# Kernel optimization log

Hardware: AMD Instinct MI355X
Metric: run time of the kernel (lower is better)

Reference implementation:

```python
import jax, jax.numpy as jnp
import numpy as np

B, C, H, W = 64, 256, 28, 28
EPS = 1e-8  # torch CosineSimilarity eps


def _make_grids(key):
    # coordinate meshgrid [2, H, W]: channel 0 = y, channel 1 = x
    yy, xx = jnp.meshgrid(jnp.arange(H, dtype=jnp.float32),
                          jnp.arange(W, dtype=jnp.float32), indexing='ij')
    coords = jnp.stack([yy, xx])  # [2, H, W]
    k1, k2 = jax.random.split(key)
    scale = jax.random.uniform(k1, (B, 1, 1, 1), minval=0.9, maxval=1.1)
    shift = jax.random.uniform(k2, (B, 2, 1, 1), minval=0.0, maxval=5.0)
    return coords[None] * scale + shift  # [B, 2, H, W]


def setup_inputs() -> dict:
    key = jax.random.key(0)
    ks = jax.random.split(key, 6)
    return {
        'y1': jax.random.normal(ks[0], (B, C, H, W), jnp.float32),
        'y2': jax.random.normal(ks[1], (B, C, H, W), jnp.float32),
        'z1': jax.random.normal(ks[2], (B, C, H, W), jnp.float32),
        'z2': jax.random.normal(ks[3], (B, C, H, W), jnp.float32),
        'view1_grid': _make_grids(ks[4]),
        'view2_grid': _make_grids(ks[5]),
    }


def _grid_distances(grid1, grid2):
    # grid*: [B, 2, H, W] -> [B, 2, N]; pairwise euclidean dist [B, N, N]
    g1 = grid1.reshape(grid1.shape[0], 2, -1)
    g2 = grid2.reshape(grid2.shape[0], 2, -1)
    dy = g1[:, 0, :, None] - g2[:, 0, None, :]
    dx = g1[:, 1, :, None] - g2[:, 1, None, :]
    return jnp.sqrt(dy * dy + dx * dx)


def _cosine_sim_pairwise(a, b):
    # a, b: [B, C, N]; cosine sim over channel dim -> [B, N, N]
    num = jnp.einsum('bcn,bcm->bnm', a, b)
    na = jnp.linalg.norm(a, axis=1)  # [B, N]
    nb = jnp.linalg.norm(b, axis=1)  # [B, N]
    den = jnp.maximum(na[:, :, None] * nb[:, None, :], EPS)
    return num / den


def _masked_mean(sim, mask):
    m = mask.astype(sim.dtype)
    return jnp.sum(sim * m) / jnp.sum(m)


def reference(y1, y2, z1, z2, view1_grid, view2_grid):
    distance_thr = 0.7
    y1f = y1.reshape(y1.shape[0], y1.shape[1], -1)
    y2f = y2.reshape(y2.shape[0], y2.shape[1], -1)
    z1f = z1.reshape(z1.shape[0], z1.shape[1], -1)
    z2f = z2.reshape(z2.shape[0], z2.shape[1], -1)

    distances = _grid_distances(view1_grid, view2_grid)  # [B, N, N]
    view1_bin = jnp.linalg.norm(view1_grid[..., 1, 1] - view1_grid[..., 0, 0], axis=-1)  # [B]
    view2_bin = jnp.linalg.norm(view2_grid[..., 1, 1] - view2_grid[..., 0, 0], axis=-1)  # [B]

    view1_mask = (distances / view1_bin[:, None, None]) <= distance_thr
    view2_mask = (distances / view2_bin[:, None, None]) <= distance_thr

    view1_loss = _masked_mean(_cosine_sim_pairwise(y1f, z2f), view1_mask)
    view2_loss = _masked_mean(_cosine_sim_pairwise(y2f, z1f), view2_mask)
    return -1.0 * (view1_loss + view2_loss)
```

## Files before the change

### kernel.cpp

```cpp
#include <hip/hip_runtime.h>
#include <hip/hip_bf16.h>

#define BB   64
#define CC   256
#define NPIX 784
#define BNP  (BB * NPIX)
#define SLOTS 128

__global__ __launch_bounds__(256) void transpose_k(
    const float* __restrict__ y1, const float* __restrict__ y2,
    const float* __restrict__ z1, const float* __restrict__ z2,
    float* __restrict__ o1, float* __restrict__ o2,
    float* __restrict__ o3, float* __restrict__ o4,
    float* __restrict__ nrm2) {
    int bx = blockIdx.x;
    int nt = bx % 13;
    int t  = bx / 13;
    int ct = t & 3;   t >>= 2;
    int b  = t & 63;
    int arr = t >> 6;

    const float* in = (arr == 0) ? y1 : (arr == 1) ? y2 : (arr == 2) ? z1 : z2;
    float* outp     = (arr == 0) ? o1 : (arr == 1) ? o2 : (arr == 2) ? o3 : o4;

    __shared__ float tile[64][65];

    int tid = threadIdx.x;
    int hi  = tid >> 4;
    int lo  = tid & 15;
    int n0  = nt * 64;
    int c0  = ct * 64;
    const float* inb = in + (size_t)b * (CC * NPIX);

#pragma unroll
    for (int k = 0; k < 4; k++) {
        int c = c0 + hi + 16 * k;
        int n = n0 + 4 * lo;
        float4 v = {0.f, 0.f, 0.f, 0.f};
        if (n < NPIX) v = *(const float4*)(inb + (size_t)c * NPIX + n);
        tile[hi + 16 * k][4 * lo + 0] = v.x;
        tile[hi + 16 * k][4 * lo + 1] = v.y;
        tile[hi + 16 * k][4 * lo + 2] = v.z;
        tile[hi + 16 * k][4 * lo + 3] = v.w;
    }
    __syncthreads();

    float* nrow = nrm2 + ((size_t)arr * BB + b) * NPIX;
#pragma unroll
    for (int k = 0; k < 4; k++) {
        int nl = hi + 16 * k;
        int n  = n0 + nl;
        float4 v;
        v.x = tile[4 * lo + 0][nl];
        v.y = tile[4 * lo + 1][nl];
        v.z = tile[4 * lo + 2][nl];
        v.w = tile[4 * lo + 3][nl];
        bool ok = (n < NPIX);
        if (ok)
            *(float4*)(outp + ((size_t)b * NPIX + n) * CC + c0 + 4 * lo) = v;
        float p = fmaf(v.x, v.x, fmaf(v.y, v.y, fmaf(v.z, v.z, v.w * v.w)));
#pragma unroll
        for (int off = 1; off < 16; off <<= 1) p += __shfl_xor(p, off);
        if (ok && lo == 0) atomicAdd(&nrow[n], p);
    }
}

__global__ __launch_bounds__(256) void pairs_k(
    const float* __restrict__ yt1, const float* __restrict__ yt2,
    const float* __restrict__ zt1, const float* __restrict__ zt2,
    const float* __restrict__ g1g, const float* __restrict__ g2g,
    const float* __restrict__ nrm2, double* __restrict__ acc) {
    int lane = threadIdx.x & 63;
    int w    = threadIdx.x >> 6;
    int wg   = blockIdx.x * 4 + w;
    int loss = (wg >= BNP) ? 1 : 0;
    int rem  = wg - loss * BNP;
    int b    = rem / NPIX;
    int i    = rem - b * NPIX;

    const float* g1 = g1g + (size_t)b * 2 * NPIX;
    const float* g2 = g2g + (size_t)b * 2 * NPIX;

    float g1y = g1[i];
    float g1x = g1[NPIX + i];

    const float* gb = loss ? g2 : g1;
    float d0  = gb[29] - gb[0];
    float d1  = gb[NPIX + 29] - gb[NPIX];
    float bin = __fsqrt_rn(__fadd_rn(__fmul_rn(d0, d0), __fmul_rn(d1, d1)));

    float t2y = g2[0], t2x = g2[NPIX];
    float s2y = g2[28] - g2[0];
    float s2x = g2[NPIX + 1] - g2[NPIX];
    float r  = 0.7f * bin * 1.0002f + 1e-4f;
    float cy = (g1y - t2y) / s2y;
    float cx = (g1x - t2x) / s2x;
    float ry = r / s2y + 0.05f;
    float rx = r / s2x + 0.05f;
    int jy0 = max(0,  (int)ceilf(cy - ry));
    int jy1 = min(27, (int)floorf(cy + ry));
    int jx0 = max(0,  (int)ceilf(cx - rx));
    int jx1 = min(27, (int)floorf(cx + rx));
    int dyr = jy1 - jy0, dxr = jx1 - jx0;

    int dyl = lane >> 2, dxl = lane & 3;
    bool pass = false;
    if (dyl <= dyr && dxl <= dxr) {
        int jc = (jy0 + dyl) * 28 + jx0 + dxl;
        float dy = g1y - g2[jc];
        float dx = g1x - g2[NPIX + jc];
        float d  = __fsqrt_rn(__fadd_rn(__fmul_rn(dy, dy), __fmul_rn(dx, dx)));
        pass = (__fdiv_rn(d, bin) <= 0.7f);
    }
    unsigned long long m = __ballot(pass);
    int cnt = __builtin_popcountll(m);

    const float* Y   = (loss ? yt2 : yt1) + ((size_t)b * NPIX + i) * CC;
    const float* Zb  = (loss ? zt1 : zt2) + (size_t)b * NPIX * CC;
    const float* zn2 = nrm2 + ((size_t)(loss ? 2 : 3) * BB + b) * NPIX;
    float yn2 = nrm2[((size_t)loss * BB + b) * NPIX + i];
    float na  = __fsqrt_rn(yn2);

    int gl = lane & 15;
    int g  = lane >> 4;

    float4 ych[4];
    if (m) {
        const float4* Y4 = (const float4*)Y;
        ych[0] = Y4[gl];
        ych[1] = Y4[gl + 16];
        ych[2] = Y4[gl + 32];
        ych[3] = Y4[gl + 48];
    }

    double ssum = 0.0;
    while (m) {
        int bt = __builtin_ctzll(m); m &= m - 1;
        int j0 = (jy0 + (bt >> 2)) * 28 + jx0 + (bt & 3);
        int j1 = j0, j2 = j0, j3 = j0;
        int nb = 1;
        if (m) {
            bt = __builtin_ctzll(m); m &= m - 1;
            j1 = (jy0 + (bt >> 2)) * 28 + jx0 + (bt & 3); nb = 2;
            if (m) {
                bt = __builtin_ctzll(m); m &= m - 1;
                j2 = (jy0 + (bt >> 2)) * 28 + jx0 + (bt & 3); nb = 3;
                if (m) {
                    bt = __builtin_ctzll(m); m &= m - 1;
                    j3 = (jy0 + (bt >> 2)) * 28 + jx0 + (bt & 3); nb = 4;
                }
            }
        }
        int js = (g == 0) ? j0 : (g == 1) ? j1 : (g == 2) ? j2 : j3;
        const float4* Z4 = (const float4*)(Zb + (size_t)js * CC);
        float4 zv0 = Z4[gl];
        float4 zv1 = Z4[gl + 16];
        float4 zv2 = Z4[gl + 32];
        float4 zv3 = Z4[gl + 48];
        float dp = ych[0].x * zv0.x;
        dp = fmaf(ych[0].y, zv0.y, dp); dp = fmaf(ych[0].z, zv0.z, dp);
        dp = fmaf(ych[0].w, zv0.w, dp);
        dp = fmaf(ych[1].x, zv1.x, dp); dp = fmaf(ych[1].y, zv1.y, dp);
        dp = fmaf(ych[1].z, zv1.z, dp); dp = fmaf(ych[1].w, zv1.w, dp);
        dp = fmaf(ych[2].x, zv2.x, dp); dp = fmaf(ych[2].y, zv2.y, dp);
        dp = fmaf(ych[2].z, zv2.z, dp); dp = fmaf(ych[2].w, zv2.w, dp);
        dp = fmaf(ych[3].x, zv3.x, dp); dp = fmaf(ych[3].y, zv3.y, dp);
        dp = fmaf(ych[3].z, zv3.z, dp); dp = fmaf(ych[3].w, zv3.w, dp);
#pragma unroll
        for (int off = 1; off < 16; off <<= 1) dp += __shfl_xor(dp, off);
        float den = fmaxf(na * __fsqrt_rn(zn2[js]), 1e-8f);
        float sim = __fdividef(dp, den);
        if (g < nb) ssum += (double)sim;
    }
    ssum += __shfl_xor(ssum, 16);
    ssum += __shfl_xor(ssum, 32);

    __shared__ double shs[4];
    __shared__ int    shc[4];
    __shared__ int    shl[4];
    if (lane == 0) { shs[w] = ssum; shc[w] = cnt; shl[w] = loss; }
    __syncthreads();
    if (threadIdx.x == 0) {
        double s[2] = {0.0, 0.0};
        double c[2] = {0.0, 0.0};
        for (int k = 0; k < 4; k++) { s[shl[k]] += shs[k]; c[shl[k]] += (double)shc[k]; }
        double* slot = acc + (size_t)(blockIdx.x & (SLOTS - 1)) * 4;
        if (s[0] != 0.0 || c[0] != 0.0) { atomicAdd(&slot[0], s[0]); atomicAdd(&slot[1], c[0]); }
        if (s[1] != 0.0 || c[1] != 0.0) { atomicAdd(&slot[2], s[1]); atomicAdd(&slot[3], c[1]); }
    }
}

__global__ void fin_k(const double* __restrict__ acc, float* __restrict__ out) {
    int lane = threadIdx.x;
    double s0 = 0, m0 = 0, s1 = 0, m1 = 0;
    for (int s = lane; s < SLOTS; s += 64) {
        const double* p = acc + (size_t)s * 4;
        s0 += p[0]; m0 += p[1]; s1 += p[2]; m1 += p[3];
    }
#pragma unroll
    for (int off = 32; off; off >>= 1) {
        s0 += __shfl_xor(s0, off); m0 += __shfl_xor(m0, off);
        s1 += __shfl_xor(s1, off); m1 += __shfl_xor(m1, off);
    }
    if (lane == 0) out[0] = (float)(-(s0 / m0 + s1 / m1));
}

extern "C" void kernel_launch(void* const* d_in, const int* in_sizes, int n_in,
                              void* d_out, int out_size, void* d_ws, size_t ws_size,
                              hipStream_t stream) {
    const float* y1 = (const float*)d_in[0];
    const float* y2 = (const float*)d_in[1];
    const float* z1 = (const float*)d_in[2];
    const float* z2 = (const float*)d_in[3];
    const float* g1 = (const float*)d_in[4];
    const float* g2 = (const float*)d_in[5];
    float* out = (float*)d_out;

    char* ws = (char*)d_ws;
    double* acc  = (double*)ws;
    float*  nrm2 = (float*)(ws + 4096);
    float*  tbase = (float*)(ws + 4096 + 4 * BNP * sizeof(float));
    const size_t E = (size_t)BB * NPIX * CC;
    float* yt1 = tbase;
    float* yt2 = tbase + E;
    float* zt1 = tbase + 2 * E;
    float* zt2 = tbase + 3 * E;

    hipMemsetAsync(ws, 0, 4096 + 4 * BNP * sizeof(float), stream);

    transpose_k<<<13312, 256, 0, stream>>>(y1, y2, z1, z2, yt1, yt2, zt1, zt2, nrm2);

    pairs_k<<<25088, 256, 0, stream>>>(yt1, yt2, zt1, zt2, g1, g2, nrm2, acc);

    fin_k<<<1, 64, 0, stream>>>(acc, out);
}
```

Before: 289.2 us.

## Transpose only z tensors and read y directly into LDS per block

The transpose kernel now handles only z1/z2, with full-channel tiles, and writes squared norms directly instead of using atomics. The memset shrinks to just the accumulator slots. pairs_k loads the four y pixels of a block straight from the NCHW layout into LDS and computes their norms in-kernel, so the y transposes and their write/read traffic are gone. The neighbor loop becomes a fixed four-round loop over 16 candidates. This cuts global memory traffic roughly in half for the preprocessing step, at the cost of a larger LDS tile with lower occupancy and an extra block barrier in pairs_k.

```diff
diff --git a/kernel.cpp b/kernel.cpp
--- a/kernel.cpp
+++ b/kernel.cpp
@@ -7,80 +7,105 @@
 #define BNP  (BB * NPIX)
 #define SLOTS 128
 
-__global__ __launch_bounds__(256) void transpose_k(
-    const float* __restrict__ y1, const float* __restrict__ y2,
+__global__ __launch_bounds__(256) void zt_k(
     const float* __restrict__ z1, const float* __restrict__ z2,
-    float* __restrict__ o1, float* __restrict__ o2,
-    float* __restrict__ o3, float* __restrict__ o4,
-    float* __restrict__ nrm2) {
+    float* __restrict__ zt, float* __restrict__ zn2) {
+    __shared__ float lds[64 * 257];
+    __shared__ float part[4][64];
+
     int bx = blockIdx.x;
     int nt = bx % 13;
     int t  = bx / 13;
-    int ct = t & 3;   t >>= 2;
     int b  = t & 63;
     int arr = t >> 6;
-
-    const float* in = (arr == 0) ? y1 : (arr == 1) ? y2 : (arr == 2) ? z1 : z2;
-    float* outp     = (arr == 0) ? o1 : (arr == 1) ? o2 : (arr == 2) ? o3 : o4;
-
-    __shared__ float tile[64][65];
-
-    int tid = threadIdx.x;
-    int hi  = tid >> 4;
-    int lo  = tid & 15;
-    int n0  = nt * 64;
-    int c0  = ct * 64;
-    const float* inb = in + (size_t)b * (CC * NPIX);
-
-#pragma unroll
-    for (int k = 0; k < 4; k++) {
-        int c = c0 + hi + 16 * k;
-        int n = n0 + 4 * lo;
+    int nlim = (nt == 12) ? 16 : 64;
+
+    const float* in = (arr ? z2 : z1) + (size_t)b * CC * NPIX + nt * 64;
+    int tid  = threadIdx.x;
+    int n4   = tid & 15;
+    int subc = tid >> 4;
+    int nn   = 4 * n4;
+
+#pragma unroll
+    for (int k = 0; k < 16; k++) {
+        int c = subc + 16 * k;
         float4 v = {0.f, 0.f, 0.f, 0.f};
-        if (n < NPIX) v = *(const float4*)(inb + (size_t)c * NPIX + n);
-        tile[hi + 16 * k][4 * lo + 0] = v.x;
-        tile[hi + 16 * k][4 * lo + 1] = v.y;
-        tile[hi + 16 * k][4 * lo + 2] = v.z;
-        tile[hi + 16 * k][4 * lo + 3] = v.w;
-    }
-    __syncthreads();
-
-    float* nrow = nrm2 + ((size_t)arr * BB + b) * NPIX;
-#pragma unroll
-    for (int k = 0; k < 4; k++) {
-        int nl = hi + 16 * k;
-        int n  = n0 + nl;
-        float4 v;
-        v.x = tile[4 * lo + 0][nl];
-        v.y = tile[4 * lo + 1][nl];
-        v.z = tile[4 * lo + 2][nl];
-        v.w = tile[4 * lo + 3][nl];
-        bool ok = (n < NPIX);
-        if (ok)
-            *(float4*)(outp + ((size_t)b * NPIX + n) * CC + c0 + 4 * lo) = v;
-        float p = fmaf(v.x, v.x, fmaf(v.y, v.y, fmaf(v.z, v.z, v.w * v.w)));
-#pragma unroll
-        for (int off = 1; off < 16; off <<= 1) p += __shfl_xor(p, off);
-        if (ok && lo == 0) atomicAdd(&nrow[n], p);
+        if (nn < nlim) v = *(const float4*)(in + (size_t)c * NPIX + nn);
+        lds[(nn + 0) * 257 + c] = v.x;
+        lds[(nn + 1) * 257 + c] = v.y;
+        lds[(nn + 2) * 257 + c] = v.z;
+        lds[(nn + 3) * 257 + c] = v.w;
+    }
+    __syncthreads();
+
+    {
+        int nl = tid & 63, cq = tid >> 6;
+        float s = 0.f;
+#pragma unroll 8
+        for (int sc = 0; sc < 64; sc++) {
+            float v = lds[nl * 257 + cq * 64 + sc];
+            s = fmaf(v, v, s);
+        }
+        part[cq][nl] = s;
+    }
+
+    float* outb = zt + ((size_t)arr * BB + b) * ((size_t)NPIX * CC)
+                     + (size_t)nt * 64 * CC;
+    int lane = tid & 63, wv = tid >> 6;
+    int c4 = lane & 15, nq = lane >> 4;
+#pragma unroll
+    for (int cq2 = 0; cq2 < 4; cq2++) {
+#pragma unroll
+        for (int nb = 0; nb < 4; nb++) {
+            int n = 16 * wv + 4 * nb + nq;
+            if (n < nlim) {
+                int cc0 = 4 * (16 * cq2 + c4);
+                float4 v;
+                v.x = lds[n * 257 + cc0 + 0];
+                v.y = lds[n * 257 + cc0 + 1];
+                v.z = lds[n * 257 + cc0 + 2];
+                v.w = lds[n * 257 + cc0 + 3];
+                *(float4*)(outb + (size_t)n * CC + cc0) = v;
+            }
+        }
+    }
+    __syncthreads();
+    if (tid < nlim) {
+        zn2[(size_t)arr * BNP + (size_t)b * NPIX + nt * 64 + tid] =
+            part[0][tid] + part[1][tid] + part[2][tid] + part[3][tid];
     }
 }
 
 __global__ __launch_bounds__(256) void pairs_k(
-    const float* __restrict__ yt1, const float* __restrict__ yt2,
-    const float* __restrict__ zt1, const float* __restrict__ zt2,
+    const float* __restrict__ y1, const float* __restrict__ y2,
+    const float* __restrict__ zt, const float* __restrict__ zn2,
     const float* __restrict__ g1g, const float* __restrict__ g2g,
-    const float* __restrict__ nrm2, double* __restrict__ acc) {
-    int lane = threadIdx.x & 63;
-    int w    = threadIdx.x >> 6;
-    int wg   = blockIdx.x * 4 + w;
-    int loss = (wg >= BNP) ? 1 : 0;
-    int rem  = wg - loss * BNP;
-    int b    = rem / NPIX;
-    int i    = rem - b * NPIX;
+    double* __restrict__ acc) {
+    __shared__ float  ylds[4 * 256];
+    __shared__ double shs[4];
+    __shared__ int    shc[4];
+
+    int tid  = threadIdx.x;
+    int lane = tid & 63, wv = tid >> 6;
+    int bx   = blockIdx.x;
+    int loss = (bx >= 12544) ? 1 : 0;
+    int rem  = bx - loss * 12544;
+    int b    = rem / 196;
+    int ig   = rem - b * 196;
+    int i0   = 4 * ig;
+
+    const float* Yg = (loss ? y2 : y1) + (size_t)b * CC * NPIX;
+    {
+        float4 v = *(const float4*)(Yg + (size_t)tid * NPIX + i0);
+        ylds[        tid] = v.x;
+        ylds[256  + tid] = v.y;
+        ylds[512  + tid] = v.z;
+        ylds[768  + tid] = v.w;
+    }
 
     const float* g1 = g1g + (size_t)b * 2 * NPIX;
     const float* g2 = g2g + (size_t)b * 2 * NPIX;
-
+    int i = i0 + wv;
     float g1y = g1[i];
     float g1x = g1[NPIX + i];
 
@@ -105,7 +130,7 @@
 
     int dyl = lane >> 2, dxl = lane & 3;
     bool pass = false;
-    if (dyl <= dyr && dxl <= dxr) {
+    if (lane < 16 && dyl <= dyr && dxl <= dxr) {
         int jc = (jy0 + dyl) * 28 + jx0 + dxl;
         float dy = g1y - g2[jc];
         float dx = g1x - g2[NPIX + jc];
@@ -115,78 +140,64 @@
     unsigned long long m = __ballot(pass);
     int cnt = __builtin_popcountll(m);
 
-    const float* Y   = (loss ? yt2 : yt1) + ((size_t)b * NPIX + i) * CC;
-    const float* Zb  = (loss ? zt1 : zt2) + (size_t)b * NPIX * CC;
-    const float* zn2 = nrm2 + ((size_t)(loss ? 2 : 3) * BB + b) * NPIX;
-    float yn2 = nrm2[((size_t)loss * BB + b) * NPIX + i];
-    float na  = __fsqrt_rn(yn2);
-
-    int gl = lane & 15;
-    int g  = lane >> 4;
-
-    float4 ych[4];
-    if (m) {
-        const float4* Y4 = (const float4*)Y;
-        ych[0] = Y4[gl];
-        ych[1] = Y4[gl + 16];
-        ych[2] = Y4[gl + 32];
-        ych[3] = Y4[gl + 48];
-    }
+    __syncthreads();
+
+    int gl = lane & 15, g = lane >> 4;
+    const float4* Yr = (const float4*)(ylds + wv * 256);
+    float4 ya = Yr[gl], yb = Yr[gl + 16], yc = Yr[gl + 32], yd = Yr[gl + 48];
+
+    float p = ya.x * ya.x;
+    p = fmaf(ya.y, ya.y, p); p = fmaf(ya.z, ya.z, p); p = fmaf(ya.w, ya.w, p);
+    p = fmaf(yb.x, yb.x, p); p = fmaf(yb.y, yb.y, p); p = fmaf(yb.z, yb.z, p);
+    p = fmaf(yb.w, yb.w, p);
+    p = fmaf(yc.x, yc.x, p); p = fmaf(yc.y, yc.y, p); p = fmaf(yc.z, yc.z, p);
+    p = fmaf(yc.w, yc.w, p);
+    p = fmaf(yd.x, yd.x, p); p = fmaf(yd.y, yd.y, p); p = fmaf(yd.z, yd.z, p);
+    p = fmaf(yd.w, yd.w, p);
+#pragma unroll
+    for (int off = 1; off < 16; off <<= 1) p += __shfl_xor(p, off);
+    float na = __fsqrt_rn(p);
+
+    const float* Zb = zt  + ((size_t)(1 - loss) * BB + b) * ((size_t)NPIX * CC);
+    const float* zn = zn2 + ((size_t)(1 - loss) * BB + b) * NPIX;
 
     double ssum = 0.0;
-    while (m) {
-        int bt = __builtin_ctzll(m); m &= m - 1;
-        int j0 = (jy0 + (bt >> 2)) * 28 + jx0 + (bt & 3);
-        int j1 = j0, j2 = j0, j3 = j0;
-        int nb = 1;
-        if (m) {
-            bt = __builtin_ctzll(m); m &= m - 1;
-            j1 = (jy0 + (bt >> 2)) * 28 + jx0 + (bt & 3); nb = 2;
-            if (m) {
-                bt = __builtin_ctzll(m); m &= m - 1;
-                j2 = (jy0 + (bt >> 2)) * 28 + jx0 + (bt & 3); nb = 3;
-                if (m) {
-                    bt = __builtin_ctzll(m); m &= m - 1;
-                    j3 = (jy0 + (bt >> 2)) * 28 + jx0 + (bt & 3); nb = 4;
-                }
-            }
-        }
-        int js = (g == 0) ? j0 : (g == 1) ? j1 : (g == 2) ? j2 : j3;
-        const float4* Z4 = (const float4*)(Zb + (size_t)js * CC);
-        float4 zv0 = Z4[gl];
-        float4 zv1 = Z4[gl + 16];
-        float4 zv2 = Z4[gl + 32];
-        float4 zv3 = Z4[gl + 48];
-        float dp = ych[0].x * zv0.x;
-        dp = fmaf(ych[0].y, zv0.y, dp); dp = fmaf(ych[0].z, zv0.z, dp);
-        dp = fmaf(ych[0].w, zv0.w, dp);
-        dp = fmaf(ych[1].x, zv1.x, dp); dp = fmaf(ych[1].y, zv1.y, dp);
-        dp = fmaf(ych[1].z, zv1.z, dp); dp = fmaf(ych[1].w, zv1.w, dp);
-        dp = fmaf(ych[2].x, zv2.x, dp); dp = fmaf(ych[2].y, zv2.y, dp);
-        dp = fmaf(ych[2].z, zv2.z, dp); dp = fmaf(ych[2].w, zv2.w, dp);
-        dp = fmaf(ych[3].x, zv3.x, dp); dp = fmaf(ych[3].y, zv3.y, dp);
-        dp = fmaf(ych[3].z, zv3.z, dp); dp = fmaf(ych[3].w, zv3.w, dp);
+#pragma unroll
+    for (int rr = 0; rr < 4; rr++) {
+        int mr = (int)((m >> (4 * rr)) & 15ull);
+        if (!mr) continue;
+        int s   = 4 * rr + g;
+        bool val = (mr >> g) & 1;
+        int j = val ? ((jy0 + (s >> 2)) * 28 + jx0 + (s & 3)) : 0;
+        const float4* Z4 = (const float4*)(Zb + (size_t)j * CC);
+        float4 za = Z4[gl], zb_ = Z4[gl + 16], zc = Z4[gl + 32], zd = Z4[gl + 48];
+        float nb2 = zn[j];
+        float dp = ya.x * za.x;
+        dp = fmaf(ya.y, za.y, dp); dp = fmaf(ya.z, za.z, dp);
+        dp = fmaf(ya.w, za.w, dp);
+        dp = fmaf(yb.x, zb_.x, dp); dp = fmaf(yb.y, zb_.y, dp);
+        dp = fmaf(yb.z, zb_.z, dp); dp = fmaf(yb.w, zb_.w, dp);
+        dp = fmaf(yc.x, zc.x, dp); dp = fmaf(yc.y, zc.y, dp);
+        dp = fmaf(yc.z, zc.z, dp); dp = fmaf(yc.w, zc.w, dp);
+        dp = fmaf(yd.x, zd.x, dp); dp = fmaf(yd.y, zd.y, dp);
+        dp = fmaf(yd.z, zd.z, dp); dp = fmaf(yd.w, zd.w, dp);
 #pragma unroll
         for (int off = 1; off < 16; off <<= 1) dp += __shfl_xor(dp, off);
-        float den = fmaxf(na * __fsqrt_rn(zn2[js]), 1e-8f);
+        float den = fmaxf(na * __fsqrt_rn(nb2), 1e-8f);
         float sim = __fdividef(dp, den);
-        if (g < nb) ssum += (double)sim;
+        if (val) ssum += (double)sim;
     }
     ssum += __shfl_xor(ssum, 16);
     ssum += __shfl_xor(ssum, 32);
 
-    __shared__ double shs[4];
-    __shared__ int    shc[4];
-    __shared__ int    shl[4];
-    if (lane == 0) { shs[w] = ssum; shc[w] = cnt; shl[w] = loss; }
-    __syncthreads();
-    if (threadIdx.x == 0) {
-        double s[2] = {0.0, 0.0};
-        double c[2] = {0.0, 0.0};
-        for (int k = 0; k < 4; k++) { s[shl[k]] += shs[k]; c[shl[k]] += (double)shc[k]; }
-        double* slot = acc + (size_t)(blockIdx.x & (SLOTS - 1)) * 4;
-        if (s[0] != 0.0 || c[0] != 0.0) { atomicAdd(&slot[0], s[0]); atomicAdd(&slot[1], c[0]); }
-        if (s[1] != 0.0 || c[1] != 0.0) { atomicAdd(&slot[2], s[1]); atomicAdd(&slot[3], c[1]); }
+    if (lane == 0) { shs[wv] = ssum; shc[wv] = cnt; }
+    __syncthreads();
+    if (tid == 0) {
+        double s = shs[0] + shs[1] + shs[2] + shs[3];
+        double c = (double)(shc[0] + shc[1] + shc[2] + shc[3]);
+        double* slot = acc + (size_t)(bx & (SLOTS - 1)) * 4;
+        atomicAdd(&slot[loss * 2],     s);
+        atomicAdd(&slot[loss * 2 + 1], c);
     }
 }
 
@@ -217,20 +228,15 @@
     float* out = (float*)d_out;
 
     char* ws = (char*)d_ws;
-    double* acc  = (double*)ws;
-    float*  nrm2 = (float*)(ws + 4096);
-    float*  tbase = (float*)(ws + 4096 + 4 * BNP * sizeof(float));
-    const size_t E = (size_t)BB * NPIX * CC;
-    float* yt1 = tbase;
-    float* yt2 = tbase + E;
-    float* zt1 = tbase + 2 * E;
-    float* zt2 = tbase + 3 * E;
-
-    hipMemsetAsync(ws, 0, 4096 + 4 * BNP * sizeof(float), stream);
-
-    transpose_k<<<13312, 256, 0, stream>>>(y1, y2, z1, z2, yt1, yt2, zt1, zt2, nrm2);
-
-    pairs_k<<<25088, 256, 0, stream>>>(yt1, yt2, zt1, zt2, g1, g2, nrm2, acc);
+    double* acc = (double*)ws;
+    float*  zn2 = (float*)(ws + 4096);
+    float*  zt  = (float*)(ws + 4096 + 2 * BNP * sizeof(float));
+
+    hipMemsetAsync(acc, 0, SLOTS * 4 * sizeof(double), stream);
+
+    zt_k<<<1664, 256, 0, stream>>>(z1, z2, zt, zn2);
+
+    pairs_k<<<25088, 256, 0, stream>>>(y1, y2, zt, zn2, g1, g2, acc);
 
     fin_k<<<1, 64, 0, stream>>>(acc, out);
 }
```

Measured after the change: 337.1 us. +16.6%, slower.
